# Optimization experiments

Hardware: AMD Instinct MI355X
Metric: run time of the kernel (lower is better)

## Reference

```python
import jax, jax.numpy as jnp
import numpy as np

HEADS = 4
D_K = 32
N_NODES = 50000
N_EDGES = 800000
IN_FEAT = 256


def setup_inputs() -> dict:
    key = jax.random.key(0)
    k1, k2, k3, k4, k5 = jax.random.split(key, 5)
    out_total = HEADS * D_K
    # xavier-uniform bound for Linear(in, out)
    bound = float(np.sqrt(6.0 / (IN_FEAT + out_total)))
    x = jax.random.normal(k1, (N_NODES, IN_FEAT), dtype=jnp.float32)
    edge_index = jax.random.randint(k2, (2, N_EDGES), 0, N_NODES, dtype=jnp.int64)
    Wq = jax.random.uniform(k3, (IN_FEAT, out_total), jnp.float32, -bound, bound)
    Wk = jax.random.uniform(k4, (IN_FEAT, out_total), jnp.float32, -bound, bound)
    Wv = jax.random.uniform(k5, (IN_FEAT, out_total), jnp.float32, -bound, bound)
    return {"x": x, "Wq": Wq, "Wk": Wk, "Wv": Wv, "edge_index": edge_index}


def reference(x, Wq, Wk, Wv, edge_index):
    n = x.shape[0]
    scale = 1.0 / np.sqrt(D_K)
    # node projections -> [N, H, D]
    Q = (x @ Wq).reshape(n, HEADS, D_K)
    K = (x @ Wk).reshape(n, HEADS, D_K)
    V = (x @ Wv).reshape(n, HEADS, D_K)
    row, col = edge_index[0], edge_index[1]
    # per-edge scaled dot-product scores [E, H]
    scores = jnp.sum(Q[row] * K[col], axis=-1) * scale
    # segment softmax keyed on destination (row)
    smax = jax.ops.segment_max(scores, row, num_segments=n)  # [N, H]
    ex = jnp.exp(scores - smax[row])
    ssum = jax.ops.segment_sum(ex, row, num_segments=n)  # [N, H]
    alpha = ex / ssum[row]  # [E, H]
    # scatter-add weighted V -> [N, H, D]
    out = jax.ops.segment_sum(alpha[:, :, None] * V[col], row, num_segments=n)
    return out.reshape(n, HEADS * D_K)
```

## Files before the change

kernel.cpp:

```cpp
#include <hip/hip_runtime.h>
#include <hip/hip_bf16.h>

#define HEADS 4
#define D_K 32
#define IN_FEAT 256
#define OUT_TOTAL (HEADS * D_K)
#define PROJ_ROWS 128
#define ELL_SLOTS 62

typedef __attribute__((ext_vector_type(8))) short bf16x8;
typedef __attribute__((ext_vector_type(4))) float f32x4;

__device__ __forceinline__ unsigned short f2bf(float f) {
    unsigned u = __float_as_uint(f);
    u += 0x7fffu + ((u >> 16) & 1u);
    return (unsigned short)(u >> 16);
}

__device__ __forceinline__ void exp8(uint4 v, float* f) {
    f[0] = __uint_as_float(v.x << 16); f[1] = __uint_as_float(v.x & 0xFFFF0000u);
    f[2] = __uint_as_float(v.y << 16); f[3] = __uint_as_float(v.y & 0xFFFF0000u);
    f[4] = __uint_as_float(v.z << 16); f[5] = __uint_as_float(v.z & 0xFFFF0000u);
    f[6] = __uint_as_float(v.w << 16); f[7] = __uint_as_float(v.w & 0xFFFF0000u);
}

__device__ __forceinline__ float dot8q(uint4 k, const float* q, float acc) {
    acc = fmaf(__uint_as_float(k.x << 16),         q[0], acc);
    acc = fmaf(__uint_as_float(k.x & 0xFFFF0000u), q[1], acc);
    acc = fmaf(__uint_as_float(k.y << 16),         q[2], acc);
    acc = fmaf(__uint_as_float(k.y & 0xFFFF0000u), q[3], acc);
    acc = fmaf(__uint_as_float(k.z << 16),         q[4], acc);
    acc = fmaf(__uint_as_float(k.z & 0xFFFF0000u), q[5], acc);
    acc = fmaf(__uint_as_float(k.w << 16),         q[6], acc);
    acc = fmaf(__uint_as_float(k.w & 0xFFFF0000u), q[7], acc);
    return acc;
}
__device__ __forceinline__ void pv8(uint4 v, float w, float* a) {
    a[0] = fmaf(__uint_as_float(v.x << 16),         w, a[0]);
    a[1] = fmaf(__uint_as_float(v.x & 0xFFFF0000u), w, a[1]);
    a[2] = fmaf(__uint_as_float(v.y << 16),         w, a[2]);
    a[3] = fmaf(__uint_as_float(v.y & 0xFFFF0000u), w, a[3]);
    a[4] = fmaf(__uint_as_float(v.z << 16),         w, a[4]);
    a[5] = fmaf(__uint_as_float(v.z & 0xFFFF0000u), w, a[5]);
    a[6] = fmaf(__uint_as_float(v.w << 16),         w, a[6]);
    a[7] = fmaf(__uint_as_float(v.w & 0xFFFF0000u), w, a[7]);
}

__global__ __launch_bounds__(256) void pack_w_kernel(
    const float* __restrict__ Wq, const float* __restrict__ Wk,
    const float* __restrict__ Wv, unsigned short* __restrict__ wt)
{
    int idx = blockIdx.x * 256 + threadIdx.x;
    if (idx >= 3 * OUT_TOTAL * IN_FEAT) return;
    int k = idx & 255;
    int c = (idx >> 8) & 127;
    int m = idx >> 15;
    const float* W = (m == 0) ? Wq : (m == 1) ? Wk : Wv;
    int ksw = k ^ ((c & 7) << 3);
    wt[(m << 15) | (c << 8) | ksw] = f2bf(W[k * OUT_TOTAL + c]);
}

__global__ __launch_bounds__(256, 3) void mega_kernel(
    const float* __restrict__ x, const unsigned short* __restrict__ wt,
    unsigned short* __restrict__ Q, unsigned short* __restrict__ K,
    unsigned short* __restrict__ V,
    const int* __restrict__ row, const int* __restrict__ col,
    unsigned short* __restrict__ ell,
    int n_nodes, int bpm, int n_edges)
{
    __shared__ unsigned short wlds[64 * IN_FEAT];

    if ((int)blockIdx.x >= bpm) {
        int e = ((int)blockIdx.x - bpm) * 256 + threadIdx.x;
        if (e < n_edges) {
            int r = row[e];
            unsigned short* rowp = ell + (size_t)r * 64;
            int pos = atomicAdd(reinterpret_cast<int*>(rowp), 1);
            if (pos < ELL_SLOTS) rowp[2 + pos] = (unsigned short)col[e];
        }
        return;
    }

    const int rb = blockIdx.x;
    const int t  = threadIdx.x;
    const int w  = t >> 6, l = t & 63;

    const int node0 = rb * PROJ_ROWS + w * 32;
    const int kc = (l >> 4) * 8;
    const int cb = l & 15;

    bf16x8 a[2][8];
#pragma unroll
    for (int rf = 0; rf < 2; rf++) {
        int r = node0 + rf * 16 + (l & 15);
        r = min(r, n_nodes - 1);
        const float* xr = x + (size_t)r * IN_FEAT + kc;
#pragma unroll
        for (int ks = 0; ks < 8; ks++) {
            float4 f0 = *reinterpret_cast<const float4*>(xr + ks * 32);
            float4 f1 = *reinterpret_cast<const float4*>(xr + ks * 32 + 4);
            bf16x8 av;
            av[0] = (short)f2bf(f0.x); av[1] = (short)f2bf(f0.y);
            av[2] = (short)f2bf(f0.z); av[3] = (short)f2bf(f0.w);
            av[4] = (short)f2bf(f1.x); av[5] = (short)f2bf(f1.y);
            av[6] = (short)f2bf(f1.z); av[7] = (short)f2bf(f1.w);
            a[rf][ks] = av;
        }
    }

    const float qscale = 0.17677669529663689f * 1.4426950408889634f;

    for (int m = 0; m < 3; m++) {
        unsigned short* __restrict__ O = (m == 0) ? Q : (m == 1) ? K : V;
#pragma unroll
        for (int half = 0; half < 2; half++) {
            __syncthreads();
            {
                const float4* src = reinterpret_cast<const float4*>(
                    wt + (size_t)m * OUT_TOTAL * IN_FEAT + half * 64 * IN_FEAT);
                float4* dst = reinterpret_cast<float4*>(wlds);
#pragma unroll
                for (int i = 0; i < 8; i++)
                    dst[i * 256 + t] = src[i * 256 + t];
            }
            __syncthreads();

            f32x4 acc[2][4];
#pragma unroll
            for (int rf = 0; rf < 2; rf++)
#pragma unroll
                for (int nfl = 0; nfl < 4; nfl++)
                    acc[rf][nfl] = (f32x4){0.f, 0.f, 0.f, 0.f};

#pragma unroll
            for (int nfl = 0; nfl < 4; nfl++) {
                const int col_local = nfl * 16 + cb;
                const int swz = (col_local & 7) << 3;
                const unsigned short* wp = &wlds[col_local * IN_FEAT];
#pragma unroll
                for (int ks = 0; ks < 8; ks++) {
                    bf16x8 b = *reinterpret_cast<const bf16x8*>(wp + ((kc + ks * 32) ^ swz));
                    acc[0][nfl] = __builtin_amdgcn_mfma_f32_16x16x32_bf16(a[0][ks], b, acc[0][nfl], 0, 0, 0);
                    acc[1][nfl] = __builtin_amdgcn_mfma_f32_16x16x32_bf16(a[1][ks], b, acc[1][nfl], 0, 0, 0);
                }
            }

#pragma unroll
            for (int rf = 0; rf < 2; rf++) {
                int r0 = node0 + rf * 16 + (l >> 4) * 4;
#pragma unroll
                for (int nfl = 0; nfl < 4; nfl++) {
                    int c = half * 64 + nfl * 16 + cb;
#pragma unroll
                    for (int j = 0; j < 4; j++) {
                        int r = r0 + j;
                        if (r < n_nodes) {
                            float v = acc[rf][nfl][j];
                            if (m == 0) v *= qscale;
                            O[(size_t)r * OUT_TOTAL + c] = f2bf(v);
                        }
                    }
                }
            }
        }
    }
}

__global__ __launch_bounds__(256) void node_attn_kernel(
    const unsigned short* __restrict__ Qb, const unsigned short* __restrict__ Kb,
    const unsigned short* __restrict__ Vb,
    const unsigned short* __restrict__ ell,
    float* __restrict__ out, int n_nodes)
{
    int wave = (blockIdx.x * 256 + threadIdx.x) >> 6;
    if (wave >= n_nodes) return;
    const int node = wave;
    const int lane = threadIdx.x & 63;
    const int h = lane & 3;
    const int slot = lane >> 2;

    const unsigned short* __restrict__ erow = ell + (size_t)node * 64;
    const int dg = min(*reinterpret_cast<const int*>(erow), ELL_SLOTS);

    float qf[32];
    {
        const uint4* qp = reinterpret_cast<const uint4*>(&Qb[(size_t)node * OUT_TOTAL + h * D_K]);
        uint4 q0 = qp[0], q1 = qp[1], q2 = qp[2], q3 = qp[3];
        exp8(q0, &qf[0]); exp8(q1, &qf[8]); exp8(q2, &qf[16]); exp8(q3, &qf[24]);
    }

    float ssum = 0.f;
    float acc[D_K];
#pragma unroll
    for (int i = 0; i < D_K; i++) acc[i] = 0.f;

    int cn = -1;
    if (dg > 0) cn = (slot < dg) ? (int)erow[2 + slot] : -1;

    for (int base = 0; base < dg; base += 16) {
        int cn_cur = cn;
        int nbase = base + 16;
        if (nbase < dg) {
            int ni = nbase + slot;
            cn = (ni < dg) ? (int)erow[2 + ni] : -1;
        }
        bool act = (cn_cur >= 0);
        int cnc = act ? cn_cur : 0;

        const uint4* kp = reinterpret_cast<const uint4*>(&Kb[(size_t)cnc * OUT_TOTAL + h * D_K]);
        const uint4* vp = reinterpret_cast<const uint4*>(&Vb[(size_t)cnc * OUT_TOTAL + h * D_K]);
        uint4 k0 = kp[0], k1 = kp[1], k2 = kp[2], k3 = kp[3];
        uint4 v0 = vp[0], v1 = vp[1], v2 = vp[2], v3 = vp[3];

        float d = 0.f;
        d = dot8q(k0, &qf[0],  d);
        d = dot8q(k1, &qf[8],  d);
        d = dot8q(k2, &qf[16], d);
        d = dot8q(k3, &qf[24], d);

        float wgt = act ? exp2f(d) : 0.f;
        ssum += wgt;

        pv8(v0, wgt, &acc[0]);
        pv8(v1, wgt, &acc[8]);
        pv8(v2, wgt, &acc[16]);
        pv8(v3, wgt, &acc[24]);
    }

    ssum += __shfl_xor(ssum, 4);
    ssum += __shfl_xor(ssum, 8);
    ssum += __shfl_xor(ssum, 16);
    ssum += __shfl_xor(ssum, 32);

    float r16[16];
    {
        const int b = (lane >> 5) & 1;
#pragma unroll
        for (int j = 0; j < 16; j++) {
            float send = b ? acc[j] : acc[j + 16];
            float keep = b ? acc[j + 16] : acc[j];
            r16[j] = keep + __shfl_xor(send, 32);
        }
    }
    float r8v[8];
    {
        const int b = (lane >> 4) & 1;
#pragma unroll
        for (int j = 0; j < 8; j++) {
            float send = b ? r16[j] : r16[j + 8];
            float keep = b ? r16[j + 8] : r16[j];
            r8v[j] = keep + __shfl_xor(send, 16);
        }
    }
    float r4[4];
    {
        const int b = (lane >> 3) & 1;
#pragma unroll
        for (int j = 0; j < 4; j++) {
            float send = b ? r8v[j] : r8v[j + 4];
            float keep = b ? r8v[j + 4] : r8v[j];
            r4[j] = keep + __shfl_xor(send, 8);
        }
    }
    float r2[2];
    {
        const int b = (lane >> 2) & 1;
#pragma unroll
        for (int j = 0; j < 2; j++) {
            float send = b ? r4[j] : r4[j + 2];
            float keep = b ? r4[j + 2] : r4[j];
            r2[j] = keep + __shfl_xor(send, 4);
        }
    }

    float inv = (ssum > 0.f) ? 1.f / ssum : 0.f;
    float2 w2;
    w2.x = r2[0] * inv;
    w2.y = r2[1] * inv;
    *reinterpret_cast<float2*>(&out[(size_t)node * OUT_TOTAL + h * D_K + slot * 2]) = w2;
}

extern "C" void kernel_launch(void* const* d_in, const int* in_sizes, int n_in,
                              void* d_out, int out_size, void* d_ws, size_t ws_size,
                              hipStream_t stream)
{
    const float* x  = (const float*)d_in[0];
    const float* Wq = (const float*)d_in[1];
    const float* Wk = (const float*)d_in[2];
    const float* Wv = (const float*)d_in[3];
    const int*   ei = (const int*)d_in[4];
    float* out = (float*)d_out;

    const int n_nodes = in_sizes[0] / IN_FEAT;
    const int n_edges = in_sizes[4] / 2;
    const int* row = ei;
    const int* col = ei + n_edges;

    char* ws = (char*)d_ws;
    unsigned short* Q = (unsigned short*)ws;  ws += (size_t)n_nodes * OUT_TOTAL * sizeof(unsigned short);
    unsigned short* K = (unsigned short*)ws;  ws += (size_t)n_nodes * OUT_TOTAL * sizeof(unsigned short);
    unsigned short* V = (unsigned short*)ws;  ws += (size_t)n_nodes * OUT_TOTAL * sizeof(unsigned short);
    unsigned short* wt = (unsigned short*)ws; ws += (size_t)3 * OUT_TOTAL * IN_FEAT * sizeof(unsigned short);
    unsigned short* ell = (unsigned short*)ws; ws += (size_t)n_nodes * 64 * sizeof(unsigned short);

    (void)hipMemsetAsync(ell, 0, (size_t)n_nodes * 64 * sizeof(unsigned short), stream);

    pack_w_kernel<<<(3 * OUT_TOTAL * IN_FEAT + 255) / 256, 256, 0, stream>>>(Wq, Wk, Wv, wt);

    int bpm = (n_nodes + PROJ_ROWS - 1) / PROJ_ROWS;
    int eb  = (n_edges + 255) / 256;
    mega_kernel<<<bpm + eb, 256, 0, stream>>>(
        x, wt, Q, K, V, row, col, ell, n_nodes, bpm, n_edges);

    node_attn_kernel<<<(n_nodes + 3) / 4, 256, 0, stream>>>(Q, K, V, ell, out, n_nodes);
}
```

Measured before the change: 120.9 us.

## Fold ELL zeroing into weight pack, split fill and projection kernels, use direct LDS loads

Replaces the separate memset with extra blocks in the weight-pack kernel that zero the ELL buffer. The fused projection+edge-fill kernel is split into a standalone fill_kernel and a proj_kernel, so the projection no longer carries the edge-fill branch. The weight tile copy into LDS now uses global_load_lds direct loads instead of going through registers. This removes one API call, but running fill and projection in sequence gives up the overlap the fused kernel had.

```diff
diff --git a/kernel.cpp b/kernel.cpp
--- a/kernel.cpp
+++ b/kernel.cpp
@@ -48,8 +48,14 @@
 
 __global__ __launch_bounds__(256) void pack_w_kernel(
     const float* __restrict__ Wq, const float* __restrict__ Wk,
-    const float* __restrict__ Wv, unsigned short* __restrict__ wt)
-{
+    const float* __restrict__ Wv, unsigned short* __restrict__ wt,
+    uint4* __restrict__ ell4, int pkb, int nz4)
+{
+    if ((int)blockIdx.x >= pkb) {
+        int i = ((int)blockIdx.x - pkb) * 256 + threadIdx.x;
+        if (i < nz4) ell4[i] = (uint4){0, 0, 0, 0};
+        return;
+    }
     int idx = blockIdx.x * 256 + threadIdx.x;
     if (idx >= 3 * OUT_TOTAL * IN_FEAT) return;
     int k = idx & 255;
@@ -60,26 +66,25 @@
     wt[(m << 15) | (c << 8) | ksw] = f2bf(W[k * OUT_TOTAL + c]);
 }
 
-__global__ __launch_bounds__(256, 3) void mega_kernel(
+__global__ __launch_bounds__(256) void fill_kernel(
+    const int* __restrict__ row, const int* __restrict__ col,
+    unsigned short* __restrict__ ell, int n_edges)
+{
+    int e = blockIdx.x * 256 + threadIdx.x;
+    if (e < n_edges) {
+        int r = row[e];
+        unsigned short* rowp = ell + (size_t)r * 64;
+        int pos = atomicAdd(reinterpret_cast<int*>(rowp), 1);
+        if (pos < ELL_SLOTS) rowp[2 + pos] = (unsigned short)col[e];
+    }
+}
+
+__global__ __launch_bounds__(256, 3) void proj_kernel(
     const float* __restrict__ x, const unsigned short* __restrict__ wt,
     unsigned short* __restrict__ Q, unsigned short* __restrict__ K,
-    unsigned short* __restrict__ V,
-    const int* __restrict__ row, const int* __restrict__ col,
-    unsigned short* __restrict__ ell,
-    int n_nodes, int bpm, int n_edges)
+    unsigned short* __restrict__ V, int n_nodes)
 {
     __shared__ unsigned short wlds[64 * IN_FEAT];
-
-    if ((int)blockIdx.x >= bpm) {
-        int e = ((int)blockIdx.x - bpm) * 256 + threadIdx.x;
-        if (e < n_edges) {
-            int r = row[e];
-            unsigned short* rowp = ell + (size_t)r * 64;
-            int pos = atomicAdd(reinterpret_cast<int*>(rowp), 1);
-            if (pos < ELL_SLOTS) rowp[2 + pos] = (unsigned short)col[e];
-        }
-        return;
-    }
 
     const int rb = blockIdx.x;
     const int t  = threadIdx.x;
@@ -116,12 +121,16 @@
         for (int half = 0; half < 2; half++) {
             __syncthreads();
             {
-                const float4* src = reinterpret_cast<const float4*>(
-                    wt + (size_t)m * OUT_TOTAL * IN_FEAT + half * 64 * IN_FEAT);
-                float4* dst = reinterpret_cast<float4*>(wlds);
-#pragma unroll
-                for (int i = 0; i < 8; i++)
-                    dst[i * 256 + t] = src[i * 256 + t];
+                const char* src = (const char*)(wt + (size_t)m * OUT_TOTAL * IN_FEAT
+                                                + half * 64 * IN_FEAT);
+                char* dstb = (char*)wlds;
+#pragma unroll
+                for (int i = 0; i < 8; i++) {
+                    __builtin_amdgcn_global_load_lds(
+                        (const __attribute__((address_space(1))) void*)(src + (i * 256 + t) * 16),
+                        (__attribute__((address_space(3))) void*)(dstb + (i * 256 + t) * 16),
+                        16, 0, 0);
+                }
             }
             __syncthreads();
 
@@ -303,14 +312,17 @@
     unsigned short* wt = (unsigned short*)ws; ws += (size_t)3 * OUT_TOTAL * IN_FEAT * sizeof(unsigned short);
     unsigned short* ell = (unsigned short*)ws; ws += (size_t)n_nodes * 64 * sizeof(unsigned short);
 
-    (void)hipMemsetAsync(ell, 0, (size_t)n_nodes * 64 * sizeof(unsigned short), stream);
-
-    pack_w_kernel<<<(3 * OUT_TOTAL * IN_FEAT + 255) / 256, 256, 0, stream>>>(Wq, Wk, Wv, wt);
+    int pkb = (3 * OUT_TOTAL * IN_FEAT + 255) / 256;
+    int nz4 = n_nodes * 8;
+    int zb  = (nz4 + 255) / 256;
+    pack_w_kernel<<<pkb + zb, 256, 0, stream>>>(Wq, Wk, Wv, wt,
+                                                (uint4*)ell, pkb, nz4);
+
+    int eb = (n_edges + 255) / 256;
+    fill_kernel<<<eb, 256, 0, stream>>>(row, col, ell, n_edges);
 
     int bpm = (n_nodes + PROJ_ROWS - 1) / PROJ_ROWS;
-    int eb  = (n_edges + 255) / 256;
-    mega_kernel<<<bpm + eb, 256, 0, stream>>>(
-        x, wt, Q, K, V, row, col, ell, n_nodes, bpm, n_edges);
+    proj_kernel<<<bpm, 256, 0, stream>>>(x, wt, Q, K, V, n_nodes);
 
     node_attn_kernel<<<(n_nodes + 3) / 4, 256, 0, stream>>>(Q, K, V, ell, out, n_nodes);
 }
```

Result: slower. 138.7 us (+14.8%).
